# Performance work log

Hardware: AMD Instinct MI355X
Metric: run time of the kernel (lower is better)

Reference implementation:

```python
import jax, jax.numpy as jnp
import numpy as np

LP_NORM = 1.2  # Lp_norm init kwarg


def setup_inputs() -> dict:
    key = jax.random.key(0)
    k0, k1, k2, k3 = jax.random.split(key, 4)
    B, L, D, H, K = 16, 1024, 512, 256, 4
    bound = np.sqrt(6.0) / np.sqrt(2.0 * H)
    x = jax.random.normal(k0, (B, L, D), dtype=jnp.float32)
    # A_selector: nn.Linear(embed_size, num_A) -> weight (K, D), bias (K,)
    W_sel = jax.random.normal(k1, (K, D), dtype=jnp.float32) * 0.02
    b_sel = jnp.zeros((K,), dtype=jnp.float32)
    # B: nn.Linear(embed_size, hidden_size, bias=False) -> weight (H, D)
    W_B = jax.random.normal(k2, (H, D), dtype=jnp.float32) * 0.02
    # A_dict: uniform in [-sqrt(6)/sqrt(2H), +sqrt(6)/sqrt(2H)], shape (H, H, K)
    A_dict = jax.random.uniform(k3, (H, H, K), dtype=jnp.float32,
                                minval=-bound, maxval=bound)
    return {"x": x, "W_sel": W_sel, "b_sel": b_sel, "W_B": W_B, "A_dict": A_dict}


def reference(x, W_sel, b_sel, W_B, A_dict):
    B, L, D = x.shape
    H = A_dict.shape[0]
    # selections = softmax(A_selector(x))  -> (B, L, K)
    sel = jax.nn.softmax(jnp.einsum('bld,kd->blk', x, W_sel) + b_sel, axis=-1)
    # inputs_ = B(x) -> (B, L, H)
    inputs_ = jnp.einsum('bld,hd->blh', x, W_B)

    def step(h, xs):
        s_t, u_t = xs  # (B, K), (B, H)
        # mix transition matrices: (H, H, K) x (B, K) -> (B, H, H)
        A = jnp.einsum('ijk,bk->bij', A_dict, s_t)
        # Lp norm over dim=1 (rows, n1), normalize columns
        norm = jnp.sum(jnp.abs(A) ** LP_NORM, axis=1) ** (1.0 / LP_NORM)  # (B, H)
        A = A / norm[:, None, :]
        h_new = jnp.einsum('bij,bj->bi', A, h) + u_t
        return h_new, h_new

    h0 = jnp.zeros((B, H), dtype=x.dtype)
    sel_t = jnp.swapaxes(sel, 0, 1)       # (L, B, K)
    inp_t = jnp.swapaxes(inputs_, 0, 1)   # (L, B, H)
    _, ys = jax.lax.scan(step, h0, (sel_t, inp_t))  # ys: (L, B, H)
    return jnp.swapaxes(ys, 0, 1)  # (B, L, H)
```

## Files before the change

### kernel.cpp

```cpp
#include <hip/hip_runtime.h>

#define B_DIM 16
#define L_DIM 1024
#define D_DIM 512
#define H_DIM 256
#define K_DIM 4

#define SLICES 8
#define RPW 32

#define OFF_HB  0
#define OFF_SEL 65536
#define OFF_RN  327680

__device__ __forceinline__ float fast_log2(float x) { return __builtin_amdgcn_logf(x); }
__device__ __forceinline__ float fast_exp2(float x) { return __builtin_amdgcn_exp2f(x); }

#define GBM 64
#define GBN 64
#define GBK 32
__global__ __launch_bounds__(256) void k_par(const float* __restrict__ x,
                                             const float* __restrict__ Wsel,
                                             const float* __restrict__ bsel,
                                             const float* __restrict__ W_B,
                                             const float* __restrict__ M,
                                             float* __restrict__ SEL,
                                             float* __restrict__ rN,
                                             float* __restrict__ out,
                                             unsigned long long* __restrict__ hb) {
    __shared__ float Xs[GBK][GBM + 1];
    __shared__ float Ws[GBK][GBN + 1];
    __shared__ float4 sel_lds[16];
    const int bid = blockIdx.x;
    const int tid = threadIdx.x;

    if (bid >= 2048) {
        for (int i = tid; i < 2 * 16 * 256; i += 256) hb[i] = 0ull;
        return;
    }

    if (bid < 1024) {
        const int b = bid >> 6;
        const int t0 = (bid & 63) << 4;
        const int lane = tid & 63;
        const int wv = tid >> 6;
        const float4* w4 = (const float4*)Wsel;
#pragma unroll
        for (int rr = 0; rr < 4; ++rr) {
            const int tt = wv * 4 + rr;
            const int row = b * L_DIM + t0 + tt;
            const float4* x4 = (const float4*)(x + (size_t)row * D_DIM);
            float4 xa = x4[lane * 2], xb = x4[lane * 2 + 1];
            float acc[4];
#pragma unroll
            for (int k = 0; k < 4; ++k) {
                float4 wa = w4[k * (D_DIM / 4) + lane * 2];
                float4 wb = w4[k * (D_DIM / 4) + lane * 2 + 1];
                acc[k] = xa.x * wa.x + xa.y * wa.y + xa.z * wa.z + xa.w * wa.w +
                         xb.x * wb.x + xb.y * wb.y + xb.z * wb.z + xb.w * wb.w;
            }
#pragma unroll
            for (int off = 1; off < 64; off <<= 1) {
#pragma unroll
                for (int k = 0; k < 4; ++k) acc[k] += __shfl_xor(acc[k], off, 64);
            }
            if (lane == 0) {
                float z[4], mx = -1e30f;
#pragma unroll
                for (int k = 0; k < 4; ++k) { z[k] = acc[k] + bsel[k]; mx = fmaxf(mx, z[k]); }
                float e[4], s = 0.0f;
#pragma unroll
                for (int k = 0; k < 4; ++k) { e[k] = fast_exp2((z[k] - mx) * 1.4426950408889634f); s += e[k]; }
                float inv = 1.0f / s;
                float4 o = { e[0] * inv, e[1] * inv, e[2] * inv, e[3] * inv };
                sel_lds[tt] = o;
                ((float4*)SEL)[row] = o;
            }
        }
        __syncthreads();

        const int j = tid;
        float s[16][4];
#pragma unroll
        for (int tt = 0; tt < 16; ++tt) {
            float4 sv = sel_lds[tt];
            s[tt][0] = sv.x; s[tt][1] = sv.y; s[tt][2] = sv.z; s[tt][3] = sv.w;
        }
        float acc[16] = {};
        const float4* M4 = (const float4*)M;
        for (int i = 0; i < H_DIM; ++i) {
            float4 m = M4[i * H_DIM + j];
#pragma unroll
            for (int tt = 0; tt < 16; ++tt) {
                float a = fmaf(m.x, s[tt][0], fmaf(m.y, s[tt][1],
                          fmaf(m.z, s[tt][2], m.w * s[tt][3])));
                a = fabsf(a);
                acc[tt] += fast_exp2(1.2f * fast_log2(a));
            }
        }
#pragma unroll
        for (int tt = 0; tt < 16; ++tt) {
            rN[(size_t)(b * L_DIM + t0 + tt) * H_DIM + j] =
                fast_exp2(-0.8333333333f * fast_log2(acc[tt]));
        }
    } else {
        const int w = bid - 1024;
        const int cb = (w & 3) * GBN;
        const int rb = (w >> 2) * GBM;
        const int tr = tid >> 4, tc = tid & 15;
        const int lrow = tid >> 2;
        const int lcol = (tid & 3) * 8;
        float acc[4][4] = {};
        for (int kt = 0; kt < D_DIM; kt += GBK) {
            float4 xa = *(const float4*)(x + (size_t)(rb + lrow) * D_DIM + kt + lcol);
            float4 xb = *(const float4*)(x + (size_t)(rb + lrow) * D_DIM + kt + lcol + 4);
            float4 wa = *(const float4*)(W_B + (size_t)(cb + lrow) * D_DIM + kt + lcol);
            float4 wb = *(const float4*)(W_B + (size_t)(cb + lrow) * D_DIM + kt + lcol + 4);
            __syncthreads();
            Xs[lcol + 0][lrow] = xa.x; Xs[lcol + 1][lrow] = xa.y;
            Xs[lcol + 2][lrow] = xa.z; Xs[lcol + 3][lrow] = xa.w;
            Xs[lcol + 4][lrow] = xb.x; Xs[lcol + 5][lrow] = xb.y;
            Xs[lcol + 6][lrow] = xb.z; Xs[lcol + 7][lrow] = xb.w;
            Ws[lcol + 0][lrow] = wa.x; Ws[lcol + 1][lrow] = wa.y;
            Ws[lcol + 2][lrow] = wa.z; Ws[lcol + 3][lrow] = wa.w;
            Ws[lcol + 4][lrow] = wb.x; Ws[lcol + 5][lrow] = wb.y;
            Ws[lcol + 6][lrow] = wb.z; Ws[lcol + 7][lrow] = wb.w;
            __syncthreads();
#pragma unroll
            for (int kk = 0; kk < GBK; ++kk) {
                float a0 = Xs[kk][tr * 4 + 0], a1 = Xs[kk][tr * 4 + 1];
                float a2 = Xs[kk][tr * 4 + 2], a3 = Xs[kk][tr * 4 + 3];
                float b0 = Ws[kk][tc * 4 + 0], b1 = Ws[kk][tc * 4 + 1];
                float b2 = Ws[kk][tc * 4 + 2], b3 = Ws[kk][tc * 4 + 3];
                acc[0][0] = fmaf(a0, b0, acc[0][0]); acc[0][1] = fmaf(a0, b1, acc[0][1]);
                acc[0][2] = fmaf(a0, b2, acc[0][2]); acc[0][3] = fmaf(a0, b3, acc[0][3]);
                acc[1][0] = fmaf(a1, b0, acc[1][0]); acc[1][1] = fmaf(a1, b1, acc[1][1]);
                acc[1][2] = fmaf(a1, b2, acc[1][2]); acc[1][3] = fmaf(a1, b3, acc[1][3]);
                acc[2][0] = fmaf(a2, b0, acc[2][0]); acc[2][1] = fmaf(a2, b1, acc[2][1]);
                acc[2][2] = fmaf(a2, b2, acc[2][2]); acc[2][3] = fmaf(a2, b3, acc[2][3]);
                acc[3][0] = fmaf(a3, b0, acc[3][0]); acc[3][1] = fmaf(a3, b1, acc[3][1]);
                acc[3][2] = fmaf(a3, b2, acc[3][2]); acc[3][3] = fmaf(a3, b3, acc[3][3]);
            }
            __syncthreads();
        }
#pragma unroll
        for (int mi = 0; mi < 4; ++mi) {
            float4 v = { acc[mi][0], acc[mi][1], acc[mi][2], acc[mi][3] };
            *(float4*)(out + (size_t)(rb + tr * 4 + mi) * H_DIM + cb + tc * 4) = v;
        }
    }
}

__global__ __launch_bounds__(256, 1) void k_scan(const float* __restrict__ M,
                                                 const float* __restrict__ SEL,
                                                 const float* __restrict__ rN,
                                                 float* __restrict__ out,
                                                 unsigned long long* hb) {
    const int wg = blockIdx.x;
    const int b = wg & 15;
    const int slice = wg >> 4;
    const int tid = threadIdx.x;
    const int q = tid >> 6;
    const int ti = tid & 63;
    const int r = ti & 31;
    const int js = ti >> 5;
    const int ig = slice * RPW + r;
    const int jbase = q * 64 + js * 32;

    float m[128];
    {
        const float4* M4 = (const float4*)M;
#pragma unroll
        for (int jj = 0; jj < 32; ++jj) {
            float4 v = M4[ig * H_DIM + jbase + jj];
            m[jj * 4 + 0] = v.x; m[jj * 4 + 1] = v.y;
            m[jj * 4 + 2] = v.z; m[jj * 4 + 3] = v.w;
        }
    }

    __shared__ float g_lds[256];
    __shared__ float part_lds[2][256];

#pragma unroll 1
    for (int t = 0; t < L_DIM; ++t) {
        float rn = rN[(size_t)(b * L_DIM + t) * H_DIM + tid];
        float4 s4 = ((const float4*)SEL)[b * L_DIM + t];
        float uval = 0.0f;
        if (tid < RPW) uval = out[(size_t)(b * L_DIM + t) * H_DIM + slice * RPW + tid];

        unsigned long long* src = hb + (size_t)(t & 1) * (16 * 256) + b * 256 + tid;
        unsigned long long w;
        while (((w = __hip_atomic_load(src, __ATOMIC_RELAXED, __HIP_MEMORY_SCOPE_AGENT)) >> 32)
               != (unsigned int)t) { }
        float h = __uint_as_float((unsigned int)w);
        g_lds[tid] = h * rn;

        float acc0 = 0, acc1 = 0, acc2 = 0, acc3 = 0;
        const float4* g4 = (const float4*)(g_lds + jbase);
#pragma unroll
        for (int jj4 = 0; jj4 < 8; ++jj4) {
            float4 gv = g4[jj4];
            acc0 = fmaf(m[(jj4 * 4 + 0) * 4 + 0], gv.x, acc0);
            acc1 = fmaf(m[(jj4 * 4 + 0) * 4 + 1], gv.x, acc1);
            acc2 = fmaf(m[(jj4 * 4 + 0) * 4 + 2], gv.x, acc2);
            acc3 = fmaf(m[(jj4 * 4 + 0) * 4 + 3], gv.x, acc3);
            acc0 = fmaf(m[(jj4 * 4 + 1) * 4 + 0], gv.y, acc0);
            acc1 = fmaf(m[(jj4 * 4 + 1) * 4 + 1], gv.y, acc1);
            acc2 = fmaf(m[(jj4 * 4 + 1) * 4 + 2], gv.y, acc2);
            acc3 = fmaf(m[(jj4 * 4 + 1) * 4 + 3], gv.y, acc3);
            acc0 = fmaf(m[(jj4 * 4 + 2) * 4 + 0], gv.z, acc0);
            acc1 = fmaf(m[(jj4 * 4 + 2) * 4 + 1], gv.z, acc1);
            acc2 = fmaf(m[(jj4 * 4 + 2) * 4 + 2], gv.z, acc2);
            acc3 = fmaf(m[(jj4 * 4 + 2) * 4 + 3], gv.z, acc3);
            acc0 = fmaf(m[(jj4 * 4 + 3) * 4 + 0], gv.w, acc0);
            acc1 = fmaf(m[(jj4 * 4 + 3) * 4 + 1], gv.w, acc1);
            acc2 = fmaf(m[(jj4 * 4 + 3) * 4 + 2], gv.w, acc2);
            acc3 = fmaf(m[(jj4 * 4 + 3) * 4 + 3], gv.w, acc3);
        }
        float part = fmaf(acc0, s4.x, fmaf(acc1, s4.y, fmaf(acc2, s4.z, acc3 * s4.w)));
        part_lds[t & 1][tid] = part;
        __syncthreads();

        if (tid < RPW) {
            float hn = uval;
#pragma unroll
            for (int p = 0; p < 8; ++p) hn += part_lds[t & 1][tid + 32 * p];
            unsigned long long pw = ((unsigned long long)(unsigned int)(t + 1) << 32) |
                                    (unsigned long long)__float_as_uint(hn);
            __hip_atomic_store(hb + (size_t)((t + 1) & 1) * (16 * 256) + b * 256 + slice * RPW + tid,
                               pw, __ATOMIC_RELAXED, __HIP_MEMORY_SCOPE_AGENT);
            out[(size_t)(b * L_DIM + t) * H_DIM + slice * RPW + tid] = hn;
        }
    }
}

extern "C" void kernel_launch(void* const* d_in, const int* in_sizes, int n_in,
                              void* d_out, int out_size, void* d_ws, size_t ws_size,
                              hipStream_t stream) {
    const float* x    = (const float*)d_in[0];
    const float* Wsel = (const float*)d_in[1];
    const float* bsel = (const float*)d_in[2];
    const float* W_B  = (const float*)d_in[3];
    const float* M    = (const float*)d_in[4];
    float* out = (float*)d_out;

    char* ws = (char*)d_ws;
    unsigned long long* hb = (unsigned long long*)(ws + OFF_HB);
    float* SEL = (float*)(ws + OFF_SEL);
    float* rN  = (float*)(ws + OFF_RN);

    k_par<<<2049, 256, 0, stream>>>(x, Wsel, bsel, W_B, M, SEL, rN, out, hb);
    k_scan<<<B_DIM * SLICES, 256, 0, stream>>>(M, SEL, rN, out, hb);
}
```

Before: 1.276 ms.

## Make each wavefront self-sufficient in scan step, replacing block barrier with shuffles

```diff
diff --git a/kernel.cpp b/kernel.cpp
--- a/kernel.cpp
+++ b/kernel.cpp
@@ -161,45 +161,58 @@
     const int slice = wg >> 4;
     const int tid = threadIdx.x;
     const int q = tid >> 6;
-    const int ti = tid & 63;
-    const int r = ti & 31;
-    const int js = ti >> 5;
-    const int ig = slice * RPW + r;
-    const int jbase = q * 64 + js * 32;
+    const int lane = tid & 63;
+    const int ro = lane & 7;
+    const int chunk = lane >> 3;
+    const int row = slice * RPW + q * 8 + ro;
+    const int jbase = chunk * 32;
 
     float m[128];
     {
         const float4* M4 = (const float4*)M;
 #pragma unroll
         for (int jj = 0; jj < 32; ++jj) {
-            float4 v = M4[ig * H_DIM + jbase + jj];
+            float4 v = M4[row * H_DIM + jbase + jj];
             m[jj * 4 + 0] = v.x; m[jj * 4 + 1] = v.y;
             m[jj * 4 + 2] = v.z; m[jj * 4 + 3] = v.w;
         }
     }
 
-    __shared__ float g_lds[256];
-    __shared__ float part_lds[2][256];
+    __shared__ float g_lds[4][2][288];
+    const int wbase = lane + ((lane >> 5) << 2);
 
 #pragma unroll 1
     for (int t = 0; t < L_DIM; ++t) {
-        float rn = rN[(size_t)(b * L_DIM + t) * H_DIM + tid];
+        const float* rnrow = rN + (size_t)(b * L_DIM + t) * H_DIM;
+        float rn0 = rnrow[lane];
+        float rn1 = rnrow[lane + 64];
+        float rn2 = rnrow[lane + 128];
+        float rn3 = rnrow[lane + 192];
         float4 s4 = ((const float4*)SEL)[b * L_DIM + t];
         float uval = 0.0f;
-        if (tid < RPW) uval = out[(size_t)(b * L_DIM + t) * H_DIM + slice * RPW + tid];
-
-        unsigned long long* src = hb + (size_t)(t & 1) * (16 * 256) + b * 256 + tid;
-        unsigned long long w;
-        while (((w = __hip_atomic_load(src, __ATOMIC_RELAXED, __HIP_MEMORY_SCOPE_AGENT)) >> 32)
-               != (unsigned int)t) { }
-        float h = __uint_as_float((unsigned int)w);
-        g_lds[tid] = h * rn;
+        if (lane < 8) uval = out[(size_t)(b * L_DIM + t) * H_DIM + row];
+
+        unsigned long long* base = hb + (size_t)(t & 1) * (16 * 256) + b * 256;
+        unsigned long long w0, w1, w2, w3;
+        const unsigned int tt = (unsigned int)t;
+        do {
+            w0 = __hip_atomic_load(base + lane,       __ATOMIC_RELAXED, __HIP_MEMORY_SCOPE_AGENT);
+            w1 = __hip_atomic_load(base + lane + 64,  __ATOMIC_RELAXED, __HIP_MEMORY_SCOPE_AGENT);
+            w2 = __hip_atomic_load(base + lane + 128, __ATOMIC_RELAXED, __HIP_MEMORY_SCOPE_AGENT);
+            w3 = __hip_atomic_load(base + lane + 192, __ATOMIC_RELAXED, __HIP_MEMORY_SCOPE_AGENT);
+        } while ((w0 >> 32) != tt || (w1 >> 32) != tt || (w2 >> 32) != tt || (w3 >> 32) != tt);
+
+        float* gw = &g_lds[q][t & 1][0];
+        gw[wbase +   0] = __uint_as_float((unsigned int)w0) * rn0;
+        gw[wbase +  72] = __uint_as_float((unsigned int)w1) * rn1;
+        gw[wbase + 144] = __uint_as_float((unsigned int)w2) * rn2;
+        gw[wbase + 216] = __uint_as_float((unsigned int)w3) * rn3;
 
         float acc0 = 0, acc1 = 0, acc2 = 0, acc3 = 0;
-        const float4* g4 = (const float4*)(g_lds + jbase);
+        const float* gr = gw + chunk * 36;
 #pragma unroll
         for (int jj4 = 0; jj4 < 8; ++jj4) {
-            float4 gv = g4[jj4];
+            float4 gv = *(const float4*)(gr + jj4 * 4);
             acc0 = fmaf(m[(jj4 * 4 + 0) * 4 + 0], gv.x, acc0);
             acc1 = fmaf(m[(jj4 * 4 + 0) * 4 + 1], gv.x, acc1);
             acc2 = fmaf(m[(jj4 * 4 + 0) * 4 + 2], gv.x, acc2);
@@ -218,18 +231,17 @@
             acc3 = fmaf(m[(jj4 * 4 + 3) * 4 + 3], gv.w, acc3);
         }
         float part = fmaf(acc0, s4.x, fmaf(acc1, s4.y, fmaf(acc2, s4.z, acc3 * s4.w)));
-        part_lds[t & 1][tid] = part;
-        __syncthreads();
-
-        if (tid < RPW) {
-            float hn = uval;
-#pragma unroll
-            for (int p = 0; p < 8; ++p) hn += part_lds[t & 1][tid + 32 * p];
-            unsigned long long pw = ((unsigned long long)(unsigned int)(t + 1) << 32) |
+        part += __shfl_xor(part, 8, 64);
+        part += __shfl_xor(part, 16, 64);
+        part += __shfl_xor(part, 32, 64);
+
+        if (lane < 8) {
+            float hn = part + uval;
+            unsigned long long pw = ((unsigned long long)(tt + 1) << 32) |
                                     (unsigned long long)__float_as_uint(hn);
-            __hip_atomic_store(hb + (size_t)((t + 1) & 1) * (16 * 256) + b * 256 + slice * RPW + tid,
+            __hip_atomic_store(hb + (size_t)((t + 1) & 1) * (16 * 256) + b * 256 + row,
                                pw, __ATOMIC_RELAXED, __HIP_MEMORY_SCOPE_AGENT);
-            out[(size_t)(b * L_DIM + t) * H_DIM + slice * RPW + tid] = hn;
+            out[(size_t)(b * L_DIM + t) * H_DIM + row] = hn;
         }
     }
 }
```

Measured after the change: 1.633 ms. 28.0% more time.

## Add L2-scoped fast-path flag buffer for cross-workgroup scan handoff

Applied to the files above, without the earlier changes.

```diff
diff --git a/kernel.cpp b/kernel.cpp
--- a/kernel.cpp
+++ b/kernel.cpp
@@ -10,11 +10,24 @@
 #define RPW 32
 
 #define OFF_HB  0
-#define OFF_SEL 65536
-#define OFF_RN  327680
+#define OFF_HBL 65536
+#define OFF_SEL 131072
+#define OFF_RN  393216
 
 __device__ __forceinline__ float fast_log2(float x) { return __builtin_amdgcn_logf(x); }
 __device__ __forceinline__ float fast_exp2(float x) { return __builtin_amdgcn_exp2f(x); }
+
+__device__ __forceinline__ unsigned long long ld_l2(const unsigned long long* p) {
+    unsigned long long r;
+    asm volatile("global_load_dwordx2 %0, %1, off sc0\n\t"
+                 "s_waitcnt vmcnt(0)"
+                 : "=&v"(r) : "v"(p) : "memory");
+    return r;
+}
+__device__ __forceinline__ void st_l2(unsigned long long* p, unsigned long long v) {
+    asm volatile("global_store_dwordx2 %0, %1, off sc0"
+                 :: "v"(p), "v"(v) : "memory");
+}
 
 #define GBM 64
 #define GBN 64
@@ -26,18 +39,12 @@
                                              const float* __restrict__ M,
                                              float* __restrict__ SEL,
                                              float* __restrict__ rN,
-                                             float* __restrict__ out,
-                                             unsigned long long* __restrict__ hb) {
+                                             float* __restrict__ out) {
     __shared__ float Xs[GBK][GBM + 1];
     __shared__ float Ws[GBK][GBN + 1];
     __shared__ float4 sel_lds[16];
     const int bid = blockIdx.x;
     const int tid = threadIdx.x;
-
-    if (bid >= 2048) {
-        for (int i = tid; i < 2 * 16 * 256; i += 256) hb[i] = 0ull;
-        return;
-    }
 
     if (bid < 1024) {
         const int b = bid >> 6;
@@ -155,7 +162,8 @@
                                                  const float* __restrict__ SEL,
                                                  const float* __restrict__ rN,
                                                  float* __restrict__ out,
-                                                 unsigned long long* hb) {
+                                                 unsigned long long* hb,
+                                                 unsigned long long* hbL) {
     const int wg = blockIdx.x;
     const int b = wg & 15;
     const int slice = wg >> 4;
@@ -167,6 +175,14 @@
     const int ig = slice * RPW + r;
     const int jbase = q * 64 + js * 32;
 
+    if (tid < RPW) {
+        const int idx = b * 256 + slice * RPW + tid;
+        st_l2(hbL + idx, 0ull);
+        st_l2(hbL + 4096 + idx, 0ull);
+        __hip_atomic_store(hb + idx, 0ull, __ATOMIC_RELAXED, __HIP_MEMORY_SCOPE_AGENT);
+        __hip_atomic_store(hb + 4096 + idx, 0ull, __ATOMIC_RELAXED, __HIP_MEMORY_SCOPE_AGENT);
+    }
+
     float m[128];
     {
         const float4* M4 = (const float4*)M;
@@ -180,6 +196,7 @@
 
     __shared__ float g_lds[256];
     __shared__ float part_lds[2][256];
+    bool fast_ok = true;
 
 #pragma unroll 1
     for (int t = 0; t < L_DIM; ++t) {
@@ -188,10 +205,23 @@
         float uval = 0.0f;
         if (tid < RPW) uval = out[(size_t)(b * L_DIM + t) * H_DIM + slice * RPW + tid];
 
-        unsigned long long* src = hb + (size_t)(t & 1) * (16 * 256) + b * 256 + tid;
-        unsigned long long w;
-        while (((w = __hip_atomic_load(src, __ATOMIC_RELAXED, __HIP_MEMORY_SCOPE_AGENT)) >> 32)
-               != (unsigned int)t) { }
+        const size_t off = (size_t)(t & 1) * (16 * 256) + b * 256 + tid;
+        const unsigned int tt = (unsigned int)t;
+        unsigned long long w = 0;
+        bool got = false;
+        if (fast_ok) {
+#pragma unroll 1
+            for (int s = 0; s < 48 && !got; ++s) {
+                w = ld_l2(hbL + off);
+                got = ((w >> 32) == tt);
+            }
+            if (!got) fast_ok = false;
+        }
+        if (!got) {
+            do {
+                w = __hip_atomic_load(hb + off, __ATOMIC_RELAXED, __HIP_MEMORY_SCOPE_AGENT);
+            } while ((w >> 32) != tt);
+        }
         float h = __uint_as_float((unsigned int)w);
         g_lds[tid] = h * rn;
 
@@ -225,10 +255,12 @@
             float hn = uval;
 #pragma unroll
             for (int p = 0; p < 8; ++p) hn += part_lds[t & 1][tid + 32 * p];
-            unsigned long long pw = ((unsigned long long)(unsigned int)(t + 1) << 32) |
+            unsigned long long pw = ((unsigned long long)(tt + 1) << 32) |
                                     (unsigned long long)__float_as_uint(hn);
-            __hip_atomic_store(hb + (size_t)((t + 1) & 1) * (16 * 256) + b * 256 + slice * RPW + tid,
-                               pw, __ATOMIC_RELAXED, __HIP_MEMORY_SCOPE_AGENT);
+            const size_t nxt = (size_t)((t + 1) & 1) * (16 * 256) + b * 256 + slice * RPW + tid;
+            st_l2(hbL + nxt, pw);
+            __hip_atomic_store(hb + nxt, pw,
+                               __ATOMIC_RELAXED, __HIP_MEMORY_SCOPE_AGENT);
             out[(size_t)(b * L_DIM + t) * H_DIM + slice * RPW + tid] = hn;
         }
     }
@@ -245,10 +277,11 @@
     float* out = (float*)d_out;
 
     char* ws = (char*)d_ws;
-    unsigned long long* hb = (unsigned long long*)(ws + OFF_HB);
+    unsigned long long* hb  = (unsigned long long*)(ws + OFF_HB);
+    unsigned long long* hbL = (unsigned long long*)(ws + OFF_HBL);
     float* SEL = (float*)(ws + OFF_SEL);
     float* rN  = (float*)(ws + OFF_RN);
 
-    k_par<<<2049, 256, 0, stream>>>(x, Wsel, bsel, W_B, M, SEL, rN, out, hb);
-    k_scan<<<B_DIM * SLICES, 256, 0, stream>>>(M, SEL, rN, out, hb);
-}
+    k_par<<<2048, 256, 0, stream>>>(x, Wsel, bsel, W_B, M, SEL, rN, out);
+    k_scan<<<B_DIM * SLICES, 256, 0, stream>>>(M, SEL, rN, out, hb, hbL);
+}
```

Result: slower. 1.318 ms (+3.3%).
